# Performance work log

Hardware: AMD Instinct MI355X
Metric: run time of the kernel (lower is better)

The kernel has to match this reference:

```python
import jax, jax.numpy as jnp
import numpy as np

R, C, H, W = 500, 512, 38, 38      # rois, VGG channels, feature-map HxW (img 608 / 16)
K, HID, POOL, SCALE = 20, 4096, 3, 16
FEAT = C * POOL * POOL             # 4608, matches fc6 in_features


def setup_inputs():
    key = jax.random.key(0)
    ks = jax.random.split(key, 12)
    fmap = jax.random.normal(ks[0], (C, H, W), dtype=jnp.float32)
    # ROIs in original image coords (x1,y1,x2,y2); width/height >= 48 px so that
    # after /16 + floor every ROI is non-degenerate (none filtered out).
    x1 = jax.random.randint(ks[1], (R,), 0, 288)
    y1 = jax.random.randint(ks[2], (R,), 0, 288)
    bw = jax.random.randint(ks[3], (R,), 48, 304)
    bh = jax.random.randint(ks[4], (R,), 48, 304)
    rois = jnp.stack([x1, y1, x1 + bw, y1 + bh], axis=1).astype(jnp.float32)
    label = jax.random.bernoulli(ks[5], 0.3, (K,)).astype(jnp.float32)
    s = 0.01
    W6 = jax.random.normal(ks[6], (FEAT, HID), jnp.float32) * s
    b6 = jnp.zeros((HID,), jnp.float32)
    W7 = jax.random.normal(ks[7], (HID, HID), jnp.float32) * s
    b7 = jnp.zeros((HID,), jnp.float32)
    W8c = jax.random.normal(ks[8], (HID, K), jnp.float32) * s
    b8c = jnp.zeros((K,), jnp.float32)
    W8d = jax.random.normal(ks[9], (HID, K), jnp.float32) * s
    b8d = jnp.zeros((K,), jnp.float32)
    return dict(fmap=fmap, rois=rois, label=label, W6=W6, b6=b6, W7=W7, b7=b7,
                W8c=W8c, b8c=b8c, W8d=W8d, b8d=b8d)


def _roi_pool(fmap, rois):
    # scaled_rois = origin_rois / 16, sliced as integer indices (floor)
    sc = jnp.floor(rois / SCALE).astype(jnp.int32)          # [R,4]
    x1, y1, x2, y2 = sc[:, 0], sc[:, 1], sc[:, 2], sc[:, 3]

    def binmask(lo, hi, size):
        # adaptive-max-pool bins: [lo + floor(j*L/3), lo + ceil((j+1)*L/3))
        L = hi - lo                                          # [R]
        j = jnp.arange(POOL)
        start = lo[:, None] + (j[None, :] * L[:, None]) // POOL
        end = lo[:, None] + (-((-(j[None, :] + 1) * L[:, None]) // POOL))
        pos = jnp.arange(size)
        return (pos[None, None, :] >= start[:, :, None]) & (pos[None, None, :] < end[:, :, None])

    cm = binmask(x1, x2, W)                                  # [R,3,W]
    rm = binmask(y1, y2, H)                                  # [R,3,H]
    neg = jnp.finfo(fmap.dtype).min
    # max over x within each x-bin: [R,C,H,3]
    tmp = jnp.max(jnp.where(cm[:, None, None, :, :], fmap[None, :, :, None, :], neg), axis=-1)
    # max over y within each y-bin: [R,C,3,3]
    pooled = jnp.max(jnp.where(rm[:, None, :, :, None], tmp[:, :, None, :, :], neg), axis=3)
    return pooled.reshape(R, FEAT), sc.astype(jnp.float32)


def _spatial_reg(scores, fc7, rois_sc, label):
    # faithful to original: argsort ascending, index 0 taken as the reference box,
    # and bboxes_iou interprets (x1,y1,x2,y2) as (x,y,w,h) — replicated as-is.
    idx = jnp.argsort(scores, axis=0)                        # [R,K]

    def per_class(idx_k, s_k, lab_k):
        h, rest = idx_k[0], idx_k[1:]
        hb = rois_sc[h]                                      # [4]
        rb = rois_sc[rest]                                   # [R-1,4]
        b1x2, b1y2 = rb[:, 0] + rb[:, 2], rb[:, 1] + rb[:, 3]
        b2x2, b2y2 = hb[0] + hb[2], hb[1] + hb[3]
        iw = jnp.clip(jnp.minimum(b1x2, b2x2) - jnp.maximum(rb[:, 0], hb[0]) + 1, 0)
        ih = jnp.clip(jnp.minimum(b1y2, b2y2) - jnp.maximum(rb[:, 1], hb[1]) + 1, 0)
        inter = iw * ih
        a1 = (b1x2 - rb[:, 0] + 1) * (b1y2 - rb[:, 1] + 1)
        a2 = (b2x2 - hb[0] + 1) * (b2y2 - hb[1] + 1)
        iou = inter / (a1 + a2 - inter)
        m = (iou > 0.6).astype(fc7.dtype)                    # [R-1]
        rf = fc7[rest] * m[:, None]
        diff = (rf - fc7[h]) * s_k[rest][:, None]
        return lab_k * 0.5 * jnp.sum(diff * diff)

    regs = jax.vmap(per_class)(idx.T, scores.T, label)       # [K]
    return jnp.sum(regs) / K


def reference(fmap, rois, label, W6, b6, W7, b7, W8c, b8c, W8d, b8d):
    feat, rois_sc = _roi_pool(fmap, rois)                    # [R,4608]
    fc6 = feat @ W6 + b6
    fc7 = fc6 @ W7 + b7
    pc = jax.nn.softmax(fc7 @ W8c + b8c, axis=1)             # per-roi over classes
    pd = jax.nn.softmax(fc7 @ W8d + b8d, axis=0)             # per-class over rois
    scores = pc * pd                                         # [R,K]
    out = jnp.sum(scores, axis=0)                            # [K], in (0,1)
    bce = -jnp.mean(label * jnp.log(out) + (1.0 - label) * jnp.log(1.0 - out))
    reg = _spatial_reg(scores, fc7, rois_sc, label)
    return scores, bce + reg, reg
```

## Files before the change

### kernel.cpp

```cpp
#include <hip/hip_runtime.h>
#include <cstdint>
#include <cstddef>

#define DEV __device__ __forceinline__

typedef __bf16 bf16_t;
typedef __bf16 bf16x8 __attribute__((ext_vector_type(8)));
typedef float  f32x4  __attribute__((ext_vector_type(4)));
typedef float  f32x2  __attribute__((ext_vector_type(2)));
typedef unsigned int u32x4 __attribute__((ext_vector_type(4)));

DEV bf16_t f2bf(float x) { return (bf16_t)x; }

constexpr int R_ = 500, C_ = 512, H_ = 38, W_ = 38, K_ = 20;
constexpr int HID = 4096, FEAT = 4608, MP = 512;
constexpr int HW = H_ * W_;

constexpr size_t alup(size_t x) { return (x + 255) & ~(size_t)255; }
constexpr size_t O_FMT  = 0;
constexpr size_t O_RSC  = alup(O_FMT  + (size_t)HW*C_*4);
constexpr size_t O_FEAT = alup(O_RSC  + (size_t)R_*4*4);
constexpr size_t O_FC6  = alup(O_FEAT + (size_t)MP*FEAT*2);
constexpr size_t O_FC7  = alup(O_FC6  + (size_t)MP*HID*2);
constexpr size_t O_PC   = alup(O_FC7  + (size_t)MP*HID*4);
constexpr size_t O_LD   = alup(O_PC   + (size_t)R_*K_*4);
constexpr size_t O_AN   = alup(O_LD   + (size_t)R_*K_*4);
constexpr size_t O_OS   = alup(O_AN   + (size_t)MP*4);
constexpr size_t O_HI   = alup(O_OS   + (size_t)K_*4);
constexpr size_t O_D    = alup(O_HI   + (size_t)K_*4);
constexpr size_t O_W8T  = alup(O_D    + (size_t)R_*K_*4);
constexpr size_t O_PART = alup(O_W8T  + (size_t)2*K_*HID*4);
constexpr size_t O_HP   = O_PART;
constexpr size_t O_DP   = O_PART + (size_t)4*1024*1024;

__global__ void __launch_bounds__(256) k_transpose(const float* __restrict__ fmap,
                                                   float* __restrict__ fmapt) {
    __shared__ float tile[32][33];
    int p0 = blockIdx.x * 32, c0 = blockIdx.y * 32;
    int tx = threadIdx.x & 31, ty = threadIdx.x >> 5;
#pragma unroll
    for (int i = 0; i < 4; ++i) {
        int c = c0 + ty + i*8, p = p0 + tx;
        tile[ty + i*8][tx] = (p < HW) ? fmap[(size_t)c*HW + p] : 0.f;
    }
    __syncthreads();
#pragma unroll
    for (int i = 0; i < 4; ++i) {
        int p = p0 + ty + i*8, c = c0 + tx;
        if (p < HW) fmapt[(size_t)p*C_ + c] = tile[tx][ty + i*8];
    }
}

__global__ void __launch_bounds__(256) k_w8t(const float* __restrict__ W8c,
                                             const float* __restrict__ W8d,
                                             float* __restrict__ W8T) {
    int k = blockIdx.x;
    const float* src = (k < K_) ? W8c : W8d;
    int kk = (k < K_) ? k : k - K_;
    for (int i = threadIdx.x; i < HID; i += 256)
        W8T[(size_t)k*HID + i] = src[(size_t)i*K_ + kk];
}

__global__ void __launch_bounds__(256) k_roipool(const float* __restrict__ fmapt,
                                                 const float* __restrict__ rois,
                                                 bf16_t* __restrict__ feat,
                                                 float* __restrict__ rois_sc) {
    int r = blockIdx.x, bin = blockIdx.y, t = threadIdx.x;
    if (r >= R_) {
        feat[(size_t)r*FEAT + (size_t)t*9       + bin] = (bf16_t)0.f;
        feat[(size_t)r*FEAT + (size_t)(t+256)*9 + bin] = (bf16_t)0.f;
        return;
    }
    int x1 = (int)floorf(rois[r*4+0] * 0.0625f);
    int y1 = (int)floorf(rois[r*4+1] * 0.0625f);
    int x2 = (int)floorf(rois[r*4+2] * 0.0625f);
    int y2 = (int)floorf(rois[r*4+3] * 0.0625f);
    if (bin == 0 && t == 0) {
        rois_sc[r*4+0] = (float)x1; rois_sc[r*4+1] = (float)y1;
        rois_sc[r*4+2] = (float)x2; rois_sc[r*4+3] = (float)y2;
    }
    int Lx = x2 - x1, Ly = y2 - y1;
    int pr = bin / 3, px = bin - pr*3;
    int rs = y1 + (pr*Ly)/3, re = y1 + ((pr+1)*Ly + 2)/3;
    int cs = x1 + (px*Lx)/3, ce = x1 + ((px+1)*Lx + 2)/3;
    float m0 = -3.402823466e38f, m1 = -3.402823466e38f;
    for (int y = rs; y < re; ++y) {
        const float* rowp = fmapt + (size_t)(y*W_)*C_;
        for (int x = cs; x < ce; ++x) {
            const float* p = rowp + (size_t)x*C_;
            m0 = fmaxf(m0, p[t]);
            m1 = fmaxf(m1, p[t + 256]);
        }
    }
    feat[(size_t)r*FEAT + (size_t)t*9       + bin] = f2bf(m0);
    feat[(size_t)r*FEAT + (size_t)(t+256)*9 + bin] = f2bf(m1);
}

__global__ void __launch_bounds__(256, 3)
k_gemm(const bf16_t* __restrict__ A, const float* __restrict__ B,
       float* __restrict__ part, int KDIM, int nts) {
    __shared__ bf16_t Asm[2][128*64];
    __shared__ bf16_t Bsm[2][64*64];
    const int t = threadIdx.x;
    const int lane = t & 63, wid = t >> 6;
    const int wr = wid >> 1, wc = wid & 1;

    const int flat = blockIdx.x + 64*blockIdx.y + 256*blockIdx.z;
    const int v = (flat & 7) * 128 + (flat >> 3);
    const int by = v & 3, bx = (v >> 2) & 63, bz = v >> 8;

    const int brow = by * 128, bcol = bx * 64;
    const int kt0 = bz * nts;

    f32x4 acc[4][2] = {};
    f32x2 br[8];
    const int n2 = t & 31, kgl = t >> 5;

    auto stage_A = [&](int kt, int buf) {
        const bf16_t* Ag = A + (size_t)brow*KDIM + kt*64;
#pragma unroll
        for (int i = 0; i < 4; ++i) {
            int s = t + i*256;
            int row = s >> 3;
            int kb = (s & 7) ^ ((row >> 1) & 7);
            const bf16_t* src = Ag + (size_t)row*KDIM + kb*8;
            bf16_t* dst = &Asm[buf][(size_t)(i*256 + (t & ~63)) * 8];
            __builtin_amdgcn_global_load_lds(
                (const __attribute__((address_space(1))) void*)src,
                (__attribute__((address_space(3))) void*)dst, 16, 0, 0);
        }
    };
    auto load_B = [&](int kt) {
        const float* src = B + (size_t)(kt*64 + kgl*8)*HID + bcol + 2*n2;
#pragma unroll
        for (int j = 0; j < 8; ++j)
            br[j] = *reinterpret_cast<const f32x2*>(src + (size_t)j*HID);
    };
    auto write_B = [&](int buf) {
        const int sw = n2 & 7;
        bf16x8 v0, v1;
#pragma unroll
        for (int j = 0; j < 8; ++j) { v0[j] = f2bf(br[j].x); v1[j] = f2bf(br[j].y); }
        *reinterpret_cast<u32x4*>(&Bsm[buf][(size_t)((2*n2    )*8 + (kgl ^ sw)) * 8]) = *reinterpret_cast<u32x4*>(&v0);
        *reinterpret_cast<u32x4*>(&Bsm[buf][(size_t)((2*n2 + 1)*8 + (kgl ^ sw)) * 8]) = *reinterpret_cast<u32x4*>(&v1);
    };

    stage_A(kt0, 0);
    load_B(kt0);
    write_B(0);
    __syncthreads();

    for (int it = 0; it < nts; ++it) {
        const int cur = it & 1;
        if (it + 1 < nts) { stage_A(kt0 + it + 1, cur ^ 1); load_B(kt0 + it + 1); }
#pragma unroll
        for (int kk = 0; kk < 2; ++kk) {
            const int kb = kk*4 + (lane >> 4);
            bf16x8 af[4], bfr[2];
#pragma unroll
            for (int m = 0; m < 4; ++m) {
                int row = wr*64 + m*16 + (lane & 15);
                af[m] = *reinterpret_cast<const bf16x8*>(
                    &Asm[cur][(size_t)(row*8 + (kb ^ ((row >> 1) & 7))) * 8]);
            }
#pragma unroll
            for (int n = 0; n < 2; ++n) {
                int nn = wc*32 + n*16 + (lane & 15);
                bfr[n] = *reinterpret_cast<const bf16x8*>(
                    &Bsm[cur][(size_t)(nn*8 + (kb ^ ((nn >> 1) & 7))) * 8]);
            }
#pragma unroll
            for (int m = 0; m < 4; ++m)
#pragma unroll
                for (int n = 0; n < 2; ++n)
                    acc[m][n] = __builtin_amdgcn_mfma_f32_16x16x32_bf16(af[m], bfr[n], acc[m][n], 0, 0, 0);
        }
        if (it + 1 < nts) { write_B(cur ^ 1); __syncthreads(); }
    }

    float* dst = part + (size_t)bz * MP * HID;
#pragma unroll
    for (int m = 0; m < 4; ++m) {
        int row0 = brow + wr*64 + m*16 + ((lane >> 4) << 2);
#pragma unroll
        for (int n = 0; n < 2; ++n) {
            int col = bcol + wc*32 + n*16 + (lane & 15);
#pragma unroll
            for (int j = 0; j < 4; ++j)
                dst[(size_t)(row0 + j)*HID + col] = acc[m][n][j];
        }
    }
}

__global__ void __launch_bounds__(256) k_reduce(const float* __restrict__ part,
                                                const float* __restrict__ bias,
                                                bf16_t* __restrict__ ob, float* __restrict__ of,
                                                int ksplit) {
    size_t idx = ((size_t)blockIdx.x*256 + threadIdx.x) * 4;
    f32x4 s = *reinterpret_cast<const f32x4*>(part + idx);
    for (int ss = 1; ss < ksplit; ++ss)
        s += *reinterpret_cast<const f32x4*>(part + (size_t)ss*MP*HID + idx);
    int col = (int)(idx & (HID - 1));
    s += *reinterpret_cast<const f32x4*>(bias + col);
    if (ob) {
#pragma unroll
        for (int j = 0; j < 4; ++j) ob[idx + j] = f2bf(s[j]);
    } else {
        *reinterpret_cast<f32x4*>(of + idx) = s;
    }
}

template<int NOUT, bool SELF>
__global__ void __launch_bounds__(256) k_dotcols(const float* __restrict__ fc7,
        const float* __restrict__ Bmat, const int* __restrict__ bidx,
        float* __restrict__ partial) {
    constexpr int NO = NOUT + (SELF ? 1 : 0);
    constexpr int SLICE = NOUT*16 + 4;
    __shared__ float Bs[8 * SLICE];
    const int rb = blockIdx.x, kb = blockIdx.y, t = threadIdx.x;
    const int k0 = kb * 128;
    for (int i = t; i < NOUT*32; i += 256) {
        int o = i >> 5, c = i & 31;
        const float* src = bidx ? fc7 + (size_t)bidx[o]*HID : Bmat + (size_t)o*HID;
        f32x4 v = *reinterpret_cast<const f32x4*>(src + k0 + c*4);
        *reinterpret_cast<f32x4*>(&Bs[(c >> 2)*SLICE + o*16 + (c & 3)*4]) = v;
    }
    __syncthreads();
    const int lane = t & 63, w = t >> 6;
    const int ri = lane >> 3, kk = lane & 7;
    const int r0 = rb*64 + w*16 + ri*2;
    f32x4 x0[4], x1[4];
    const float* f0 = fc7 + (size_t)r0*HID + k0 + kk*16;
#pragma unroll
    for (int j = 0; j < 4; ++j) {
        x0[j] = *reinterpret_cast<const f32x4*>(f0 + j*4);
        x1[j] = *reinterpret_cast<const f32x4*>(f0 + HID + j*4);
    }
    float acc0[NO], acc1[NO];
#pragma unroll
    for (int o = 0; o < NOUT; ++o) {
        f32x4 s0 = {}, s1 = {};
#pragma unroll
        for (int j = 0; j < 4; ++j) {
            f32x4 wv = *reinterpret_cast<const f32x4*>(&Bs[kk*SLICE + o*16 + j*4]);
            s0 += x0[j] * wv;
            s1 += x1[j] * wv;
        }
        acc0[o] = s0[0]+s0[1]+s0[2]+s0[3];
        acc1[o] = s1[0]+s1[1]+s1[2]+s1[3];
    }
    if (SELF) {
        f32x4 s0 = {}, s1 = {};
#pragma unroll
        for (int j = 0; j < 4; ++j) { s0 += x0[j]*x0[j]; s1 += x1[j]*x1[j]; }
        acc0[NO-1] = s0[0]+s0[1]+s0[2]+s0[3];
        acc1[NO-1] = s1[0]+s1[1]+s1[2]+s1[3];
    }
#pragma unroll
    for (int o = 0; o < NO; ++o) {
#pragma unroll
        for (int m = 1; m < 8; m <<= 1) {
            acc0[o] += __shfl_xor(acc0[o], m, 64);
            acc1[o] += __shfl_xor(acc1[o], m, 64);
        }
    }
    if (kk == 0) {
#pragma unroll
        for (int o = 0; o < NO; ++o) {
            partial[((size_t)kb*MP + r0    )*NO + o] = acc0[o];
            partial[((size_t)kb*MP + r0 + 1)*NO + o] = acc1[o];
        }
    }
}

__global__ void __launch_bounds__(64) k_headred(const float* __restrict__ hpart,
        const float* __restrict__ b8c, const float* __restrict__ b8d,
        float* __restrict__ pc, float* __restrict__ ld, float* __restrict__ An) {
    int r = blockIdx.x, t = threadIdx.x;
    __shared__ float lcs[20];
    if (t < 41) {
        float s = 0.f;
        for (int kb = 0; kb < 32; ++kb) s += hpart[((size_t)kb*MP + r)*41 + t];
        if (t < 20)      lcs[t] = s + b8c[t];
        else if (t < 40) ld[r*K_ + (t-20)] = s + b8d[t-20];
        else             An[r] = s;
    }
    __syncthreads();
    if (t == 0) {
        float mx = lcs[0];
#pragma unroll
        for (int k = 1; k < 20; ++k) mx = fmaxf(mx, lcs[k]);
        float sum = 0.f, e[20];
#pragma unroll
        for (int k = 0; k < 20; ++k) { e[k] = expf(lcs[k] - mx); sum += e[k]; }
        float inv = 1.f / sum;
#pragma unroll
        for (int k = 0; k < 20; ++k) pc[r*K_ + k] = e[k] * inv;
    }
}

__global__ void __launch_bounds__(64) k_dmatred(const float* __restrict__ dpart,
                                                float* __restrict__ D) {
    int r = blockIdx.x, t = threadIdx.x;
    if (t < 20) {
        float s = 0.f;
        for (int kb = 0; kb < 32; ++kb) s += dpart[((size_t)kb*MP + r)*20 + t];
        D[r*K_ + t] = s;
    }
}

__global__ void __launch_bounds__(256) k_pd(const float* __restrict__ ld,
        const float* __restrict__ pc, float* __restrict__ scores,
        float* __restrict__ out_sum, int* __restrict__ h_idx) {
    int k = blockIdx.x, t = threadIdx.x;
    __shared__ float sh[4];
    float m = -3.402823466e38f;
    for (int r = t; r < R_; r += 256) m = fmaxf(m, ld[r*K_ + k]);
    for (int off = 1; off < 64; off <<= 1) m = fmaxf(m, __shfl_xor(m, off, 64));
    if ((t & 63) == 0) sh[t >> 6] = m;
    __syncthreads();
    m = fmaxf(fmaxf(sh[0], sh[1]), fmaxf(sh[2], sh[3]));
    __syncthreads();
    float s = 0.f;
    for (int r = t; r < R_; r += 256) s += expf(ld[r*K_ + k] - m);
    for (int off = 1; off < 64; off <<= 1) s += __shfl_xor(s, off, 64);
    if ((t & 63) == 0) sh[t >> 6] = s;
    __syncthreads();
    s = sh[0] + sh[1] + sh[2] + sh[3];
    float inv = 1.f / s;

    float osum = 0.f, bv = 3.402823466e38f; int bi = 0x7fffffff;
    for (int r = t; r < R_; r += 256) {
        float p  = expf(ld[r*K_ + k] - m) * inv;
        float sc = pc[r*K_ + k] * p;
        scores[r*K_ + k] = sc;
        osum += sc;
        if (sc < bv || (sc == bv && r < bi)) { bv = sc; bi = r; }
    }
    for (int off = 1; off < 64; off <<= 1) osum += __shfl_xor(osum, off, 64);
    for (int off = 1; off < 64; off <<= 1) {
        float v2 = __shfl_xor(bv, off, 64);
        int   i2 = __shfl_xor(bi, off, 64);
        if (v2 < bv || (v2 == bv && i2 < bi)) { bv = v2; bi = i2; }
    }
    __shared__ float so[4], mv[4]; __shared__ int mi[4];
    if ((t & 63) == 0) { so[t >> 6] = osum; mv[t >> 6] = bv; mi[t >> 6] = bi; }
    __syncthreads();
    if (t == 0) {
        out_sum[k] = so[0] + so[1] + so[2] + so[3];
        float v = mv[0]; int i = mi[0];
        for (int w = 1; w < 4; ++w)
            if (mv[w] < v || (mv[w] == v && mi[w] < i)) { v = mv[w]; i = mi[w]; }
        h_idx[k] = i;
    }
}

__global__ void __launch_bounds__(256) k_final(const float* __restrict__ out_sum,
        const int* __restrict__ h_idx, const float* __restrict__ label,
        const float* __restrict__ scores, const float* __restrict__ D,
        const float* __restrict__ An, const float* __restrict__ rois_sc,
        float* __restrict__ dout) {
    int t = threadIdx.x;
    __shared__ float bsh[20];
    if (t < 20) {
        float o = out_sum[t], lab = label[t];
        bsh[t] = lab * logf(o) + (1.f - lab) * logf(1.f - o);
    }
    __syncthreads();

    float rp = 0.f;
    for (int i = t; i < R_*K_; i += 256) {
        int r = i / 20, k = i - r*20;
        int h = h_idx[k];
        if (r == h) continue;
        float lab = label[k];
        if (lab == 0.f) continue;
        float s = scores[r*K_ + k];
        const float* rb = rois_sc + r*4;
        const float* hb = rois_sc + h*4;
        float b1x2 = rb[0] + rb[2], b1y2 = rb[1] + rb[3];
        float b2x2 = hb[0] + hb[2], b2y2 = hb[1] + hb[3];
        float iw = fmaxf(fminf(b1x2, b2x2) - fmaxf(rb[0], hb[0]) + 1.f, 0.f);
        float ih = fmaxf(fminf(b1y2, b2y2) - fmaxf(rb[1], hb[1]) + 1.f, 0.f);
        float inter = iw * ih;
        float a1 = (b1x2 - rb[0] + 1.f) * (b1y2 - rb[1] + 1.f);
        float a2 = (b2x2 - hb[0] + 1.f) * (b2y2 - hb[1] + 1.f);
        float iou = inter / (a1 + a2 - inter);
        float mm = (iou > 0.6f) ? 1.f : 0.f;
        float term = mm * (An[r] - 2.f * D[r*K_ + k]) + An[h];
        rp += lab * 0.5f * s * s * term;
    }
    for (int off = 1; off < 64; off <<= 1) rp += __shfl_xor(rp, off, 64);
    __shared__ float rsh[4];
    if ((t & 63) == 0) rsh[t >> 6] = rp;
    __syncthreads();
    if (t == 0) {
        float reg = (rsh[0] + rsh[1] + rsh[2] + rsh[3]) / (float)K_;
        float b = 0.f;
        for (int k = 0; k < 20; ++k) b += bsh[k];
        float bce = -b / (float)K_;
        dout[R_*K_]     = bce + reg;
        dout[R_*K_ + 1] = reg;
    }
}

extern "C" void kernel_launch(void* const* d_in, const int* in_sizes, int n_in,
                              void* d_out, int out_size, void* d_ws, size_t ws_size,
                              hipStream_t stream) {
    const float* fmap  = (const float*)d_in[0];
    const float* rois  = (const float*)d_in[1];
    const float* label = (const float*)d_in[2];
    const float* W6    = (const float*)d_in[3];
    const float* b6    = (const float*)d_in[4];
    const float* W7    = (const float*)d_in[5];
    const float* b7    = (const float*)d_in[6];
    const float* W8c   = (const float*)d_in[7];
    const float* b8c   = (const float*)d_in[8];
    const float* W8d   = (const float*)d_in[9];
    const float* b8d   = (const float*)d_in[10];
    char* ws = (char*)d_ws;
    float* out = (float*)d_out;

    float*  fmapt = (float*)(ws + O_FMT);
    float*  roisc = (float*)(ws + O_RSC);
    bf16_t* feat  = (bf16_t*)(ws + O_FEAT);
    bf16_t* fc6   = (bf16_t*)(ws + O_FC6);
    float*  fc7   = (float*)(ws + O_FC7);
    float*  pc    = (float*)(ws + O_PC);
    float*  ld    = (float*)(ws + O_LD);
    float*  An    = (float*)(ws + O_AN);
    float*  osum  = (float*)(ws + O_OS);
    int*    hidx  = (int*)(ws + O_HI);
    float*  Dm    = (float*)(ws + O_D);
    float*  w8t   = (float*)(ws + O_W8T);
    float*  part  = (float*)(ws + O_PART);
    float*  hpart = (float*)(ws + O_HP);
    float*  dpart = (float*)(ws + O_DP);

    const int ksplit = 4;

    k_transpose<<<dim3((HW + 31)/32, C_/32), dim3(256), 0, stream>>>(fmap, fmapt);
    k_w8t      <<<dim3(2*K_),   dim3(256), 0, stream>>>(W8c, W8d, w8t);
    k_roipool  <<<dim3(MP, 9),  dim3(256), 0, stream>>>(fmapt, rois, feat, roisc);

    k_gemm  <<<dim3(HID/64, MP/128, ksplit), dim3(256), 0, stream>>>(feat, W6, part, FEAT, (FEAT/64)/ksplit);
    k_reduce<<<dim3((MP*HID)/1024), dim3(256), 0, stream>>>(part, b6, fc6, (float*)nullptr, ksplit);

    k_gemm  <<<dim3(HID/64, MP/128, ksplit), dim3(256), 0, stream>>>(fc6, W7, part, HID, (HID/64)/ksplit);
    k_reduce<<<dim3((MP*HID)/1024), dim3(256), 0, stream>>>(part, b7, (bf16_t*)nullptr, fc7, ksplit);

    k_dotcols<40, true><<<dim3(MP/64, HID/128), dim3(256), 0, stream>>>(fc7, w8t, (const int*)nullptr, hpart);
    k_headred<<<dim3(R_), dim3(64), 0, stream>>>(hpart, b8c, b8d, pc, ld, An);
    k_pd     <<<dim3(K_), dim3(256), 0, stream>>>(ld, pc, out, osum, hidx);
    k_dotcols<20, false><<<dim3(MP/64, HID/128), dim3(256), 0, stream>>>(fc7, (const float*)nullptr, hidx, dpart);
    k_dmatred<<<dim3(R_), dim3(64), 0, stream>>>(dpart, Dm);
    k_final  <<<dim3(1),  dim3(256), 0, stream>>>(osum, hidx, label, out, Dm, An, roisc, out);
}
```

Measured before the change: 199.1 us.

## Widen GEMM tiles to 128x128 and pre-transpose W7 to bf16 for LDS-direct loads

Both FC GEMMs now use 128x128 output tiles instead of 128x64, with occupancy hint lowered to 2 blocks per CU and a matching grid swizzle. This raises MFMA work per LDS byte and halves the number of blocks that re-read each B column. A new prep kernel merges the fmap transpose and the W8 transpose, and also converts W7 to a transposed bf16 copy. That copy lets the fc7 GEMM stage both operands with global_load_lds instead of fp32 register loads plus conversion. The trade-off is an extra full pass over the 64 MB W7 on every call, and lower occupancy.

```diff
diff --git a/kernel.cpp b/kernel.cpp
--- a/kernel.cpp
+++ b/kernel.cpp
@@ -15,6 +15,7 @@
 constexpr int R_ = 500, C_ = 512, H_ = 38, W_ = 38, K_ = 20;
 constexpr int HID = 4096, FEAT = 4608, MP = 512;
 constexpr int HW = H_ * W_;
+constexpr int KSPLIT = 4;
 
 constexpr size_t alup(size_t x) { return (x + 255) & ~(size_t)255; }
 constexpr size_t O_FMT  = 0;
@@ -29,36 +30,60 @@
 constexpr size_t O_HI   = alup(O_OS   + (size_t)K_*4);
 constexpr size_t O_D    = alup(O_HI   + (size_t)K_*4);
 constexpr size_t O_W8T  = alup(O_D    + (size_t)R_*K_*4);
-constexpr size_t O_PART = alup(O_W8T  + (size_t)2*K_*HID*4);
+constexpr size_t O_W7T  = alup(O_W8T  + (size_t)2*K_*HID*4);
+constexpr size_t O_PART = alup(O_W7T  + (size_t)HID*HID*2);
 constexpr size_t O_HP   = O_PART;
 constexpr size_t O_DP   = O_PART + (size_t)4*1024*1024;
 
-__global__ void __launch_bounds__(256) k_transpose(const float* __restrict__ fmap,
-                                                   float* __restrict__ fmapt) {
-    __shared__ float tile[32][33];
-    int p0 = blockIdx.x * 32, c0 = blockIdx.y * 32;
-    int tx = threadIdx.x & 31, ty = threadIdx.x >> 5;
-#pragma unroll
-    for (int i = 0; i < 4; ++i) {
-        int c = c0 + ty + i*8, p = p0 + tx;
-        tile[ty + i*8][tx] = (p < HW) ? fmap[(size_t)c*HW + p] : 0.f;
-    }
-    __syncthreads();
-#pragma unroll
-    for (int i = 0; i < 4; ++i) {
-        int p = p0 + ty + i*8, c = c0 + tx;
-        if (p < HW) fmapt[(size_t)p*C_ + c] = tile[tx][ty + i*8];
-    }
-}
-
-__global__ void __launch_bounds__(256) k_w8t(const float* __restrict__ W8c,
-                                             const float* __restrict__ W8d,
-                                             float* __restrict__ W8T) {
-    int k = blockIdx.x;
-    const float* src = (k < K_) ? W8c : W8d;
-    int kk = (k < K_) ? k : k - K_;
-    for (int i = threadIdx.x; i < HID; i += 256)
-        W8T[(size_t)k*HID + i] = src[(size_t)i*K_ + kk];
+__global__ void __launch_bounds__(256) k_prep(const float* __restrict__ fmap,
+                                              float* __restrict__ fmapt,
+                                              const float* __restrict__ W8c,
+                                              const float* __restrict__ W8d,
+                                              float* __restrict__ W8T,
+                                              const float* __restrict__ W7,
+                                              bf16_t* __restrict__ W7T) {
+    int b = blockIdx.x, t = threadIdx.x;
+    if (b < 736) {
+        __shared__ float tile[32][33];
+        int p0 = (b % 46) * 32, c0 = (b / 46) * 32;
+        int tx = t & 31, ty = t >> 5;
+#pragma unroll
+        for (int i = 0; i < 4; ++i) {
+            int c = c0 + ty + i*8, p = p0 + tx;
+            tile[ty + i*8][tx] = (p < HW) ? fmap[(size_t)c*HW + p] : 0.f;
+        }
+        __syncthreads();
+#pragma unroll
+        for (int i = 0; i < 4; ++i) {
+            int p = p0 + ty + i*8, c = c0 + tx;
+            if (p < HW) fmapt[(size_t)p*C_ + c] = tile[tx][ty + i*8];
+        }
+    } else if (b < 776) {
+        int k = b - 736;
+        const float* src = (k < K_) ? W8c : W8d;
+        int kk = (k < K_) ? k : k - K_;
+        for (int i = t; i < HID; i += 256)
+            W8T[(size_t)k*HID + i] = src[(size_t)i*K_ + kk];
+    } else {
+        __shared__ float tile[64][65];
+        int j = b - 776;
+        int k0 = (j >> 6) * 64, n0 = (j & 63) * 64;
+#pragma unroll
+        for (int i = 0; i < 16; ++i) {
+            int idx = t + i*256;
+            int kk = idx >> 6, nn = idx & 63;
+            tile[kk][nn] = W7[(size_t)(k0 + kk)*HID + n0 + nn];
+        }
+        __syncthreads();
+#pragma unroll
+        for (int i = 0; i < 8; ++i) {
+            int idx = t + i*256;
+            int nn = idx >> 5, kw = idx & 31;
+            bf16_t a = f2bf(tile[2*kw][nn]), c = f2bf(tile[2*kw + 1][nn]);
+            unsigned int u = ((unsigned short*)&a)[0] | ((unsigned int)((unsigned short*)&c)[0] << 16);
+            *reinterpret_cast<unsigned int*>(&W7T[(size_t)(n0 + nn)*HID + k0 + 2*kw]) = u;
+        }
+    }
 }
 
 __global__ void __launch_bounds__(256) k_roipool(const float* __restrict__ fmapt,
@@ -96,25 +121,26 @@
     feat[(size_t)r*FEAT + (size_t)(t+256)*9 + bin] = f2bf(m1);
 }
 
-__global__ void __launch_bounds__(256, 3)
+__global__ void __launch_bounds__(256, 2)
 k_gemm(const bf16_t* __restrict__ A, const float* __restrict__ B,
        float* __restrict__ part, int KDIM, int nts) {
     __shared__ bf16_t Asm[2][128*64];
-    __shared__ bf16_t Bsm[2][64*64];
+    __shared__ bf16_t Bsm[2][128*64];
     const int t = threadIdx.x;
     const int lane = t & 63, wid = t >> 6;
     const int wr = wid >> 1, wc = wid & 1;
 
-    const int flat = blockIdx.x + 64*blockIdx.y + 256*blockIdx.z;
-    const int v = (flat & 7) * 128 + (flat >> 3);
-    const int by = v & 3, bx = (v >> 2) & 63, bz = v >> 8;
-
-    const int brow = by * 128, bcol = bx * 64;
+    const int flat = blockIdx.x + 32*blockIdx.y + 128*blockIdx.z;
+    const int q = 16 * gridDim.z;
+    const int v = (flat & 7) * q + (flat >> 3);
+    const int by = v & 3, bx = (v >> 2) & 31, bz = v >> 7;
+
+    const int brow = by * 128, bcol = bx * 128;
     const int kt0 = bz * nts;
 
-    f32x4 acc[4][2] = {};
-    f32x2 br[8];
-    const int n2 = t & 31, kgl = t >> 5;
+    f32x4 acc[4][4] = {};
+    f32x2 br[16];
+    const int n2 = t & 63, kgl = t >> 6;
 
     auto stage_A = [&](int kt, int buf) {
         const bf16_t* Ag = A + (size_t)brow*KDIM + kt*64;
@@ -131,18 +157,22 @@
         }
     };
     auto load_B = [&](int kt) {
-        const float* src = B + (size_t)(kt*64 + kgl*8)*HID + bcol + 2*n2;
-#pragma unroll
-        for (int j = 0; j < 8; ++j)
+        const float* src = B + (size_t)(kt*64 + kgl*16)*HID + bcol + 2*n2;
+#pragma unroll
+        for (int j = 0; j < 16; ++j)
             br[j] = *reinterpret_cast<const f32x2*>(src + (size_t)j*HID);
     };
     auto write_B = [&](int buf) {
         const int sw = n2 & 7;
         bf16x8 v0, v1;
 #pragma unroll
-        for (int j = 0; j < 8; ++j) { v0[j] = f2bf(br[j].x); v1[j] = f2bf(br[j].y); }
-        *reinterpret_cast<u32x4*>(&Bsm[buf][(size_t)((2*n2    )*8 + (kgl ^ sw)) * 8]) = *reinterpret_cast<u32x4*>(&v0);
-        *reinterpret_cast<u32x4*>(&Bsm[buf][(size_t)((2*n2 + 1)*8 + (kgl ^ sw)) * 8]) = *reinterpret_cast<u32x4*>(&v1);
+        for (int j = 0; j < 8; ++j) { v0[j] = f2bf(br[j].x); v1[j] = f2bf(br[j+8].x); }
+        *reinterpret_cast<u32x4*>(&Bsm[buf][(size_t)((2*n2)*8 + ((kgl*2    ) ^ sw)) * 8]) = *reinterpret_cast<u32x4*>(&v0);
+        *reinterpret_cast<u32x4*>(&Bsm[buf][(size_t)((2*n2)*8 + ((kgl*2 + 1) ^ sw)) * 8]) = *reinterpret_cast<u32x4*>(&v1);
+#pragma unroll
+        for (int j = 0; j < 8; ++j) { v0[j] = f2bf(br[j].y); v1[j] = f2bf(br[j+8].y); }
+        *reinterpret_cast<u32x4*>(&Bsm[buf][(size_t)((2*n2+1)*8 + ((kgl*2    ) ^ sw)) * 8]) = *reinterpret_cast<u32x4*>(&v0);
+        *reinterpret_cast<u32x4*>(&Bsm[buf][(size_t)((2*n2+1)*8 + ((kgl*2 + 1) ^ sw)) * 8]) = *reinterpret_cast<u32x4*>(&v1);
     };
 
     stage_A(kt0, 0);
@@ -156,7 +186,7 @@
 #pragma unroll
         for (int kk = 0; kk < 2; ++kk) {
             const int kb = kk*4 + (lane >> 4);
-            bf16x8 af[4], bfr[2];
+            bf16x8 af[4], bfr[4];
 #pragma unroll
             for (int m = 0; m < 4; ++m) {
                 int row = wr*64 + m*16 + (lane & 15);
@@ -164,15 +194,15 @@
                     &Asm[cur][(size_t)(row*8 + (kb ^ ((row >> 1) & 7))) * 8]);
             }
 #pragma unroll
-            for (int n = 0; n < 2; ++n) {
-                int nn = wc*32 + n*16 + (lane & 15);
+            for (int n = 0; n < 4; ++n) {
+                int nn = wc*64 + n*16 + (lane & 15);
                 bfr[n] = *reinterpret_cast<const bf16x8*>(
                     &Bsm[cur][(size_t)(nn*8 + (kb ^ ((nn >> 1) & 7))) * 8]);
             }
 #pragma unroll
             for (int m = 0; m < 4; ++m)
 #pragma unroll
-                for (int n = 0; n < 2; ++n)
+                for (int n = 0; n < 4; ++n)
                     acc[m][n] = __builtin_amdgcn_mfma_f32_16x16x32_bf16(af[m], bfr[n], acc[m][n], 0, 0, 0);
         }
         if (it + 1 < nts) { write_B(cur ^ 1); __syncthreads(); }
@@ -183,8 +213,94 @@
     for (int m = 0; m < 4; ++m) {
         int row0 = brow + wr*64 + m*16 + ((lane >> 4) << 2);
 #pragma unroll
-        for (int n = 0; n < 2; ++n) {
-            int col = bcol + wc*32 + n*16 + (lane & 15);
+        for (int n = 0; n < 4; ++n) {
+            int col = bcol + wc*64 + n*16 + (lane & 15);
+#pragma unroll
+            for (int j = 0; j < 4; ++j)
+                dst[(size_t)(row0 + j)*HID + col] = acc[m][n][j];
+        }
+    }
+}
+
+__global__ void __launch_bounds__(256, 2)
+k_gemm_bt(const bf16_t* __restrict__ A, const bf16_t* __restrict__ BT,
+          float* __restrict__ part, int KDIM, int nts) {
+    __shared__ bf16_t Asm[2][128*64];
+    __shared__ bf16_t Bsm[2][128*64];
+    const int t = threadIdx.x;
+    const int lane = t & 63, wid = t >> 6;
+    const int wr = wid >> 1, wc = wid & 1;
+
+    const int flat = blockIdx.x + 32*blockIdx.y + 128*blockIdx.z;
+    const int q = 16 * gridDim.z;
+    const int v = (flat & 7) * q + (flat >> 3);
+    const int by = v & 3, bx = (v >> 2) & 31, bz = v >> 7;
+
+    const int brow = by * 128, bcol = bx * 128;
+    const int kt0 = bz * nts;
+
+    f32x4 acc[4][4] = {};
+
+    auto stage = [&](const bf16_t* base, int kt, bf16_t* lds) {
+        const bf16_t* g = base + kt*64;
+#pragma unroll
+        for (int i = 0; i < 4; ++i) {
+            int s = t + i*256;
+            int row = s >> 3;
+            int kb = (s & 7) ^ ((row >> 1) & 7);
+            const bf16_t* src = g + (size_t)row*KDIM + kb*8;
+            bf16_t* dst = lds + (size_t)(i*256 + (t & ~63)) * 8;
+            __builtin_amdgcn_global_load_lds(
+                (const __attribute__((address_space(1))) void*)src,
+                (__attribute__((address_space(3))) void*)dst, 16, 0, 0);
+        }
+    };
+
+    const bf16_t* Abase = A  + (size_t)brow*KDIM;
+    const bf16_t* Bbase = BT + (size_t)bcol*KDIM;
+
+    stage(Abase, kt0, &Asm[0][0]);
+    stage(Bbase, kt0, &Bsm[0][0]);
+    __syncthreads();
+
+    for (int it = 0; it < nts; ++it) {
+        const int cur = it & 1;
+        if (it + 1 < nts) {
+            stage(Abase, kt0 + it + 1, &Asm[cur ^ 1][0]);
+            stage(Bbase, kt0 + it + 1, &Bsm[cur ^ 1][0]);
+        }
+#pragma unroll
+        for (int kk = 0; kk < 2; ++kk) {
+            const int kb = kk*4 + (lane >> 4);
+            bf16x8 af[4], bfr[4];
+#pragma unroll
+            for (int m = 0; m < 4; ++m) {
+                int row = wr*64 + m*16 + (lane & 15);
+                af[m] = *reinterpret_cast<const bf16x8*>(
+                    &Asm[cur][(size_t)(row*8 + (kb ^ ((row >> 1) & 7))) * 8]);
+            }
+#pragma unroll
+            for (int n = 0; n < 4; ++n) {
+                int nn = wc*64 + n*16 + (lane & 15);
+                bfr[n] = *reinterpret_cast<const bf16x8*>(
+                    &Bsm[cur][(size_t)(nn*8 + (kb ^ ((nn >> 1) & 7))) * 8]);
+            }
+#pragma unroll
+            for (int m = 0; m < 4; ++m)
+#pragma unroll
+                for (int n = 0; n < 4; ++n)
+                    acc[m][n] = __builtin_amdgcn_mfma_f32_16x16x32_bf16(af[m], bfr[n], acc[m][n], 0, 0, 0);
+        }
+        __syncthreads();
+    }
+
+    float* dst = part + (size_t)bz * MP * HID;
+#pragma unroll
+    for (int m = 0; m < 4; ++m) {
+        int row0 = brow + wr*64 + m*16 + ((lane >> 4) << 2);
+#pragma unroll
+        for (int n = 0; n < 4; ++n) {
+            int col = bcol + wc*64 + n*16 + (lane & 15);
 #pragma unroll
             for (int j = 0; j < 4; ++j)
                 dst[(size_t)(row0 + j)*HID + col] = acc[m][n][j];
@@ -433,21 +549,19 @@
     int*    hidx  = (int*)(ws + O_HI);
     float*  Dm    = (float*)(ws + O_D);
     float*  w8t   = (float*)(ws + O_W8T);
+    bf16_t* w7t   = (bf16_t*)(ws + O_W7T);
     float*  part  = (float*)(ws + O_PART);
     float*  hpart = (float*)(ws + O_HP);
     float*  dpart = (float*)(ws + O_DP);
 
-    const int ksplit = 4;
-
-    k_transpose<<<dim3((HW + 31)/32, C_/32), dim3(256), 0, stream>>>(fmap, fmapt);
-    k_w8t      <<<dim3(2*K_),   dim3(256), 0, stream>>>(W8c, W8d, w8t);
-    k_roipool  <<<dim3(MP, 9),  dim3(256), 0, stream>>>(fmapt, rois, feat, roisc);
-
-    k_gemm  <<<dim3(HID/64, MP/128, ksplit), dim3(256), 0, stream>>>(feat, W6, part, FEAT, (FEAT/64)/ksplit);
-    k_reduce<<<dim3((MP*HID)/1024), dim3(256), 0, stream>>>(part, b6, fc6, (float*)nullptr, ksplit);
-
-    k_gemm  <<<dim3(HID/64, MP/128, ksplit), dim3(256), 0, stream>>>(fc6, W7, part, HID, (HID/64)/ksplit);
-    k_reduce<<<dim3((MP*HID)/1024), dim3(256), 0, stream>>>(part, b7, (bf16_t*)nullptr, fc7, ksplit);
+    k_prep   <<<dim3(776 + 4096), dim3(256), 0, stream>>>(fmap, fmapt, W8c, W8d, w8t, W7, w7t);
+    k_roipool<<<dim3(MP, 9),      dim3(256), 0, stream>>>(fmapt, rois, feat, roisc);
+
+    k_gemm   <<<dim3(HID/128, MP/128, KSPLIT), dim3(256), 0, stream>>>(feat, W6, part, FEAT, (FEAT/64)/KSPLIT);
+    k_reduce <<<dim3((MP*HID)/1024), dim3(256), 0, stream>>>(part, b6, fc6, (float*)nullptr, KSPLIT);
+
+    k_gemm_bt<<<dim3(HID/128, MP/128, KSPLIT), dim3(256), 0, stream>>>(fc6, w7t, part, HID, (HID/64)/KSPLIT);
+    k_reduce <<<dim3((MP*HID)/1024), dim3(256), 0, stream>>>(part, b7, (bf16_t*)nullptr, fc7, KSPLIT);
 
     k_dotcols<40, true><<<dim3(MP/64, HID/128), dim3(256), 0, stream>>>(fc7, w8t, (const int*)nullptr, hpart);
     k_headred<<<dim3(R_), dim3(64), 0, stream>>>(hpart, b8c, b8d, pc, ld, An);
```

Measured after the change: 182.4 us. 1.09x faster.
